# Kernel optimization log

Hardware: AMD Instinct MI355X
Metric: run time of the kernel (lower is better)

The kernel has to match this reference:

```python
import jax, jax.numpy as jnp
import numpy as np

N, H, DK, DV, DFF, D = 2, 8, 32, 32, 512, 256
B, S = 2, 2048
MASK_VALUE = -1e-30
EPS = 1e-14  # K.epsilon()**2 with default epsilon 1e-7


def glorot(key, shape):
    fan_in, fan_out = shape[-2], shape[-1]
    limit = np.sqrt(6.0 / (fan_in + fan_out))
    return jax.random.uniform(key, shape, jnp.float32, -limit, limit)


def setup_inputs() -> dict:
    key = jax.random.key(0)
    ks = jax.random.split(key, 8)
    return {
        "x": jax.random.normal(ks[0], (B, S, D), jnp.float32),
        "mask": jnp.ones((B, S), jnp.float32),
        "Wq": glorot(ks[1], (N, H, D, DK)),
        "Wk": glorot(ks[2], (N, H, D, DK)),
        "Wv": glorot(ks[3], (N, H, D, DV)),
        "Wo": glorot(ks[4], (N, H * DV, D)),
        "W1": glorot(ks[5], (N, D, DFF)),
        "b1": jnp.zeros((N, DFF), jnp.float32),
        "W2": glorot(ks[6], (N, DFF, D)),
        "b2": jnp.zeros((N, D), jnp.float32),
        "gamma": jnp.ones((2 * N,), jnp.float32),
        "beta": jnp.zeros((2 * N,), jnp.float32),
    }


def _layernorm(x, g, b):
    mean = jnp.mean(x, axis=-1, keepdims=True)
    var = jnp.mean(jnp.square(x - mean), axis=-1, keepdims=True)
    return (x - mean) / jnp.sqrt(var + EPS) * g + b


def reference(x, mask, Wq, Wk, Wv, Wo, W1, b1, W2, b2, gamma, beta):
    m = mask[:, None, None, :]  # [B,1,1,S], multiplies score rows' key axis
    for i in range(N):
        # batched multi-head attention (no 1/sqrt(dk) scaling, faithful to source)
        q = jnp.einsum("bsd,hdk->bhsk", x, Wq[i])
        k = jnp.einsum("bsd,hdk->bhsk", x, Wk[i])
        v = jnp.einsum("bsd,hdv->bhsv", x, Wv[i])
        A = jnp.einsum("bhsk,bhtk->bhst", q, k)  # [B,H,S,S]
        A = m * A + (1.0 - m) * MASK_VALUE
        A = jax.nn.softmax(A, axis=-1)
        o = jnp.einsum("bhst,bhtv->bhsv", A, v)
        conc = o.transpose(0, 2, 1, 3).reshape(x.shape[0], x.shape[1], H * DV)
        x = x + conc @ Wo[i]
        x = _layernorm(x, gamma[2 * i], beta[2 * i])
        ffn = jax.nn.relu(x @ W1[i] + b1[i]) @ W2[i] + b2[i]
        x = x + ffn
        x = _layernorm(x, gamma[2 * i + 1], beta[2 * i + 1])
    return x
```

## Files before the change

### kernel.cpp

```cpp
#include <hip/hip_runtime.h>
#include <hip/hip_bf16.h>

#define NL 2
#define NH 8
#define DKk 32
#define DVv 32
#define DFF 512
#define DD 256
#define BB 2
#define SS 2048
#define MROWS (BB*SS)
#define LN_EPS 1e-14f
#define L2E 1.4426950408889634f
#define SOFT_SHIFT_L2E (50.0f*L2E)

typedef __hip_bfloat16 bf16;
typedef unsigned short us;
typedef short bf16x8 __attribute__((ext_vector_type(8)));
typedef float f32x4  __attribute__((ext_vector_type(4)));
typedef unsigned short us4 __attribute__((ext_vector_type(4)));

#define O_XF   256
#define O_QB   (O_XF+1048576)
#define O_KH   (O_QB+1048576)
#define O_KL   (O_KH+524288)
#define O_VT   (O_KL+524288)
#define O_XH   (O_VT+524288)
#define O_XL   (O_XH+524288)
#define O_OP   (O_XL+524288)
#define O_ML   (O_OP+2097152)
#define O_MASK (O_ML+65536)
#define O_B1   (O_MASK+4096)
#define O_B2   (O_B1+1024)
#define O_GM   (O_B2+512)
#define O_BT   (O_GM+4)
#define O_PREP (O_BT+4)
#define TAIL_TOTAL (4096+1024+512+4+4)
#define CONV_BLOCKS (512 + (TAIL_TOTAL+255)/256)
#define PREP_BLOCKS 512
#define PQH 0u
#define PQL 393216u
#define POH 786432u
#define POL 917504u
#define P1H 1048576u
#define P1L 1310720u
#define P2H 1572864u
#define P2L 1835008u

__device__ __forceinline__ float us2f(us u){
  unsigned int v = ((unsigned int)u) << 16; float f;
  __builtin_memcpy(&f, &v, 4); return f;
}
__device__ __forceinline__ us f2bf_rne(float f){
  unsigned int b = __float_as_uint(f);
  b += 0x7FFFu + ((b>>16)&1u);
  return (us)(b>>16);
}

#if __has_builtin(__builtin_amdgcn_exp2f)
#define EXP2F(x) __builtin_amdgcn_exp2f(x)
#else
#define EXP2F(x) exp2f(x)
#endif

#if __has_builtin(__builtin_amdgcn_cvt_pk_bf16_f32)
typedef __bf16 bf16x2_t __attribute__((ext_vector_type(2)));
__device__ __forceinline__ int pack_bf16(float a, float b){
  bf16x2_t r = __builtin_amdgcn_cvt_pk_bf16_f32(a, b);
  int i; __builtin_memcpy(&i, &r, 4); return i;
}
#else
__device__ __forceinline__ int pack_bf16(float a, float b){
  int b0 = __float_as_int(a) + 0x8000;
  int b1 = __float_as_int(b) + 0x8000;
  return (b1 & 0xFFFF0000) | ((int)((unsigned)b0 >> 16));
}
#endif

__device__ __forceinline__ void gl_lds16(const us* g, us* l){
  __builtin_amdgcn_global_load_lds(
    (const __attribute__((address_space(1))) unsigned int*)g,
    (__attribute__((address_space(3))) unsigned int*)l, 16, 0, 0);
}

__device__ __forceinline__ size_t xhl_idx(int row, int col){
  int rt = row>>6, rg = (row>>4)&3, L15 = row&15;
  int kc = col>>5, Q = (col>>3)&3, j = col&7;
  return ((size_t)(rt*8+kc))*2048 + rg*512 + Q*128 + L15*8 + j;
}

__device__ __forceinline__ float conv1(const void* src, size_t i, int flag){
  if(flag) return ((const float*)src)[i];
  return us2f(((const us*)src)[i]);
}

__device__ __forceinline__ void prep_b_raw(const void* W0, const void* W1v, const void* W2v,
                                           int baseoff, us* __restrict__ Bh, us* __restrict__ Bl,
                                           int Kd, int Nd, int qkv, int g, int flag)
{
  int total = (Kd/32)*(Nd/16)*64;
  if(g >= total) return;
  int lane = g & 63, fi = g >> 6;
  int ncN = Nd/16;
  int nc = fi % ncN, kc = fi / ncN;
  int Q = lane>>4, L15 = lane&15;
  int n = nc*16 + L15;
  const void* src;
  int off0, stride;
  if(qkv){
    int sec = n>>8, h = (n>>5)&7, kq = n&31;
    src = (sec==0)?W0:((sec==1)?W1v:W2v);
    off0 = baseoff + h*8192 + kq;
    stride = 32;
  } else {
    src = W0;
    off0 = baseoff + n;
    stride = Nd;
  }
  #pragma unroll
  for(int j=0;j<8;j++){
    int k = kc*32 + Q*8 + j;
    float v = conv1(src, (size_t)off0 + (size_t)k*stride, flag);
    us hb = f2bf_rne(v);
    Bh[(size_t)g*8 + j] = hb;
    Bl[(size_t)g*8 + j] = f2bf_rne(v - us2f(hb));
  }
}

__global__ void conv_prep(const void* s0, const void* s1, const void* sWq, const void* sWk,
                          const void* sWv, const void* sWo, const void* sW1, const void* sb1,
                          const void* sW2, const void* sb2, const void* sgm, const void* sbt,
                          float* __restrict__ ws, int* __restrict__ flagp)
{
  __shared__ int fsh[4];
  int bad = 0;
  const us* xr = (const us*)s0;
  for(int i=threadIdx.x; i<4096; i+=256){
    float f = us2f(xr[i]);
    if(!(fabsf(f) < 1e3f)) bad = 1;
  }
  unsigned long long m = __ballot(bad);
  if((threadIdx.x&63)==0) fsh[threadIdx.x>>6] = (m!=0ull);
  __syncthreads();
  int flag = (fsh[0]|fsh[1]|fsh[2]|fsh[3]);
  if(blockIdx.x==0 && threadIdx.x==0) *flagp = flag;

  int b = blockIdx.x;
  if(b < PREP_BLOCKS){
    int layer = b >> 8, lb = b & 255;
    us* prep = (us*)(ws + O_PREP);
    if(lb < 96){
      int g = lb*256 + threadIdx.x;
      prep_b_raw(sWq, sWk, sWv, layer*65536, prep+PQH+(size_t)layer*196608,
                 prep+PQL+(size_t)layer*196608, 256, 768, 1, g, flag);
    } else if(lb < 128){
      int g = (lb-96)*256 + threadIdx.x;
      prep_b_raw(sWo, nullptr, nullptr, layer*65536, prep+POH+(size_t)layer*65536,
                 prep+POL+(size_t)layer*65536, 256, 256, 0, g, flag);
    } else if(lb < 192){
      int g = (lb-128)*256 + threadIdx.x;
      prep_b_raw(sW1, nullptr, nullptr, layer*131072, prep+P1H+(size_t)layer*131072,
                 prep+P1L+(size_t)layer*131072, 256, 512, 0, g, flag);
    } else {
      int g = (lb-192)*256 + threadIdx.x;
      prep_b_raw(sW2, nullptr, nullptr, layer*131072, prep+P2H+(size_t)layer*131072,
                 prep+P2L+(size_t)layer*131072, 512, 256, 0, g, flag);
    }
    return;
  }
  int b2 = b - PREP_BLOCKS;
  if(b2 < 512){
    int g8 = b2*256 + threadIdx.x;
    int e0 = g8*8;
    float v[8];
    if(flag){
      float4 a0 = *((const float4*)s0 + (e0>>2));
      float4 a1 = *((const float4*)s0 + (e0>>2) + 1);
      v[0]=a0.x; v[1]=a0.y; v[2]=a0.z; v[3]=a0.w;
      v[4]=a1.x; v[5]=a1.y; v[6]=a1.z; v[7]=a1.w;
    } else {
      bf16x8 u = *((const bf16x8*)s0 + g8);
      #pragma unroll
      for(int j=0;j<8;j++) v[j] = us2f((us)u[j]);
    }
    *(float4*)&ws[O_XF+e0]   = (float4){v[0],v[1],v[2],v[3]};
    *(float4*)&ws[O_XF+e0+4] = (float4){v[4],v[5],v[6],v[7]};
    union{ us a[8]; uint4 q; } hh, ll;
    #pragma unroll
    for(int j=0;j<8;j++){
      us hb = f2bf_rne(v[j]);
      hh.a[j] = hb;
      ll.a[j] = f2bf_rne(v[j] - us2f(hb));
    }
    size_t xi = xhl_idx(e0>>8, e0&255);
    *(uint4*)&((us*)(ws+O_XH))[xi] = hh.q;
    *(uint4*)&((us*)(ws+O_XL))[xi] = ll.q;
    return;
  }
  int g = (b2-512)*256 + threadIdx.x;
  if(g < 4096){ ws[O_MASK+g] = conv1(s1, g, flag)*L2E; return; }
  g -= 4096;
  if(g < 1024){ ws[O_B1+g] = conv1(sb1, g, flag); return; }
  g -= 1024;
  if(g < 512){ ws[O_B2+g] = conv1(sb2, g, flag); return; }
  g -= 512;
  if(g < 4){ ws[O_GM+g] = conv1(sgm, g, flag); return; }
  g -= 4;
  if(g < 4){ ws[O_BT+g] = conv1(sbt, g, flag); return; }
}

template<int MODE>
__launch_bounds__(256)
__global__ void gemm_mfma(const us* __restrict__ Axh, const us* __restrict__ Axl,
                          const us* __restrict__ Bh, const us* __restrict__ Bl,
                          const float* __restrict__ bias,
                          float* __restrict__ O,
                          us* __restrict__ QH, us* __restrict__ QL,
                          us* __restrict__ KH, us* __restrict__ KL, us* __restrict__ VT,
                          int Ncols, int Kdim)
{
  __shared__ __align__(16) us SH[16384];
  const int t = threadIdx.x;
  const int w = t>>6, lane = t&63;
  const int Q = lane>>4, L15 = lane&15;
  const int bx = blockIdx.x, by = blockIdx.y;
  const int row0 = bx*64;
  const int nc0 = by*4;
  const int col0 = by*64;
  const int nKc = Kdim>>5;
  const int ncW = Ncols>>4;

  f32x4 acc[2][2];
  #pragma unroll
  for(int i=0;i<2;i++)
    #pragma unroll
    for(int j=0;j<2;j++) acc[i][j] = (f32x4){0.f,0.f,0.f,0.f};

  auto stage = [&](int kc){
    const int bo = (kc&1)*8192;
    size_t abase = ((size_t)(bx*nKc + kc))*2048;
    gl_lds16(&Axh[abase + (size_t)t*8], &SH[bo + t*8]);
    gl_lds16(&Axl[abase + (size_t)t*8], &SH[bo + 2048 + t*8]);
    size_t gidx = ((size_t)(kc*ncW + nc0 + w)*64 + lane)*8;
    gl_lds16(&Bh[gidx], &SH[bo + 4096 + t*8]);
    gl_lds16(&Bl[gidx], &SH[bo + 6144 + t*8]);
  };

  stage(0);

  for(int kc=0; kc<nKc; kc++){
    __syncthreads();
    if(kc+1 < nKc) stage(kc+1);
    const int bo = (kc&1)*8192;
    const us* Ah  = SH + bo;
    const us* Al  = SH + bo + 2048;
    const us* Bhs = SH + bo + 4096;
    const us* Bls = SH + bo + 6144;

    bf16x8 aAh[2], aAl[2], bBh[2], bBl[2];
    #pragma unroll
    for(int rg2=0;rg2<2;rg2++){
      int rg = (w&1)*2 + rg2;
      aAh[rg2] = *(const bf16x8*)&Ah[rg*512 + lane*8];
      aAl[rg2] = *(const bf16x8*)&Al[rg*512 + lane*8];
    }
    #pragma unroll
    for(int cg2=0;cg2<2;cg2++){
      int nc = (w>>1)*2 + cg2;
      bBh[cg2] = *(const bf16x8*)&Bhs[nc*512 + lane*8];
      bBl[cg2] = *(const bf16x8*)&Bls[nc*512 + lane*8];
    }
    #pragma unroll
    for(int rg2=0;rg2<2;rg2++)
      #pragma unroll
      for(int cg2=0;cg2<2;cg2++){
        acc[rg2][cg2] = __builtin_amdgcn_mfma_f32_16x16x32_bf16(aAl[rg2], bBh[cg2], acc[rg2][cg2], 0,0,0);
        acc[rg2][cg2] = __builtin_amdgcn_mfma_f32_16x16x32_bf16(aAh[rg2], bBl[cg2], acc[rg2][cg2], 0,0,0);
        acc[rg2][cg2] = __builtin_amdgcn_mfma_f32_16x16x32_bf16(aAh[rg2], bBh[cg2], acc[rg2][cg2], 0,0,0);
      }
  }

  if(MODE==0){
    __syncthreads();
    us* TH = SH;
    us* TL = SH + 4608;
    #pragma unroll
    for(int rg2=0;rg2<2;rg2++)
      #pragma unroll
      for(int cg2=0;cg2<2;cg2++)
        #pragma unroll
        for(int r=0;r<4;r++){
          int rl = (w&1)*32 + rg2*16 + Q*4 + r;
          int cl = (w>>1)*32 + cg2*16 + L15;
          float va = acc[rg2][cg2][r];
          us hb = f2bf_rne(va);
          TH[rl*72+cl] = hb;
          TL[rl*72+cl] = f2bf_rne(va - us2f(hb));
        }
    __syncthreads();
    const int sec = col0>>8;
    const int h0  = (col0&255)>>5;
    const int b_  = row0>>11;
    const int srow0 = row0 & 2047;
    if(sec < 2){
      us* DH = (sec==0) ? QH : KH;
      us* DL = (sec==0) ? QL : KL;
      #pragma unroll
      for(int u2=0; u2<2; u2++){
        int u = w + u2*4;
        int rg = u&3, half = u>>2;
        int lbase = (rg*16 + L15)*72 + half*32 + Q*8;
        bf16x8 hv = *(const bf16x8*)&TH[lbase];
        bf16x8 lv = *(const bf16x8*)&TL[lbase];
        int bh = b_*NH + h0 + half;
        size_t dbase = ((size_t)(bh*128 + (srow0>>4) + rg)*64 + lane)*8;
        *(bf16x8*)&DH[dbase] = hv;
        *(bf16x8*)&DL[dbase] = lv;
      }
    } else {
      #pragma unroll
      for(int u2=0; u2<2; u2++){
        int u = w + u2*4;
        int sgrp = u&1, kqh = (u>>1)&1, half = u>>2;
        union{ us u8[8]; bf16x8 v; } vv;
        #pragma unroll
        for(int j=0;j<8;j++){
          int rl = sgrp*32 + Q*8 + j;
          int cl = half*32 + kqh*16 + L15;
          vv.u8[j] = TH[rl*72+cl];
        }
        int bh = b_*NH + h0 + half;
        size_t dbase = ((size_t)((bh*64 + (srow0>>5) + sgrp)*2 + kqh)*64 + lane)*8;
        *(bf16x8*)&VT[dbase] = vv.v;
      }
    }
  } else {
    #pragma unroll
    for(int rg2=0;rg2<2;rg2++)
      #pragma unroll
      for(int cg2=0;cg2<2;cg2++)
        #pragma unroll
        for(int r=0;r<4;r++){
          int row = row0 + (w&1)*32 + rg2*16 + Q*4 + r;
          int c   = col0 + (w>>1)*32 + cg2*16 + L15;
          float v = acc[rg2][cg2][r] + bias[c];
          O[(size_t)row*Ncols + c] = v>0.f ? v : 0.f;
        }
  }
}

__launch_bounds__(256)
__global__ void oln_ffn(const float* __restrict__ OpartA, const float* __restrict__ MLA,
                        const us* __restrict__ WOh, const us* __restrict__ WOl,
                        const us* __restrict__ W1h, const us* __restrict__ W1l,
                        const us* __restrict__ W2h, const us* __restrict__ W2l,
                        const float* __restrict__ b1, const float* __restrict__ b2,
                        float* __restrict__ xf, us* __restrict__ xh, us* __restrict__ xl,
                        const float* __restrict__ gamma, const float* __restrict__ beta, int gi0,
                        void* __restrict__ out, int write_out, const int* __restrict__ flagp)
{
  __shared__ __align__(16) us xAH[4096], xAL[4096];
  __shared__ __align__(16) us hAH[8192], hAL[8192];
  __shared__ float lred[128];
  const int t = threadIdx.x;
  const int w = t>>6, lane = t&63;
  const int Q = lane>>4, L15 = lane&15;
  const int row0 = blockIdx.x*16;
  const int b_ = row0>>11, s0_ = row0&2047;

  f32x4 acc[4];
  #pragma unroll
  for(int cg=0;cg<4;cg++) acc[cg] = (f32x4){0.f,0.f,0.f,0.f};

  #pragma unroll 2
  for(int kc=0; kc<8; kc++){
    size_t i0 = ((size_t)(b_*8 + kc))*2048 + s0_ + L15;
    float l0 = MLA[i0], l1 = MLA[i0+32768];
    float inv = 1.f/(l0 + l1);
    const float* p0 = &OpartA[i0*32 + Q*8];
    const float* p1 = &OpartA[(i0+32768)*32 + Q*8];
    float4 a0 = *(const float4*)p0, a1 = *(const float4*)(p0+4);
    float4 c0 = *(const float4*)p1, c1 = *(const float4*)(p1+4);
    float fv[8];
    fv[0]=(a0.x+c0.x)*inv; fv[1]=(a0.y+c0.y)*inv; fv[2]=(a0.z+c0.z)*inv; fv[3]=(a0.w+c0.w)*inv;
    fv[4]=(a1.x+c1.x)*inv; fv[5]=(a1.y+c1.y)*inv; fv[6]=(a1.z+c1.z)*inv; fv[7]=(a1.w+c1.w)*inv;
    union{ us a[8]; bf16x8 v; } Ahv, Alv;
    #pragma unroll
    for(int j=0;j<8;j++){
      us hb = f2bf_rne(fv[j]);
      Ahv.a[j] = hb;
      Alv.a[j] = f2bf_rne(fv[j] - us2f(hb));
    }
    #pragma unroll
    for(int cg=0;cg<4;cg++){
      size_t fi = (size_t)(kc*16 + w*4 + cg)*512 + (size_t)lane*8;
      bf16x8 bBh = *(const bf16x8*)&WOh[fi];
      bf16x8 bBl = *(const bf16x8*)&WOl[fi];
      acc[cg] = __builtin_amdgcn_mfma_f32_16x16x32_bf16(Alv.v, bBh, acc[cg], 0,0,0);
      acc[cg] = __builtin_amdgcn_mfma_f32_16x16x32_bf16(Ahv.v, bBl, acc[cg], 0,0,0);
      acc[cg] = __builtin_amdgcn_mfma_f32_16x16x32_bf16(Ahv.v, bBh, acc[cg], 0,0,0);
    }
  }

  float tmp[4][4];
  #pragma unroll
  for(int cg=0;cg<4;cg++)
    #pragma unroll
    for(int r=0;r<4;r++){
      int row = row0 + Q*4 + r;
      int c = w*64 + cg*16 + L15;
      tmp[cg][r] = acc[cg][r] + xf[(size_t)row*DD + c];
    }
  float s[4], sq[4];
  #pragma unroll
  for(int r=0;r<4;r++){
    s[r]  = tmp[0][r]+tmp[1][r]+tmp[2][r]+tmp[3][r];
    sq[r] = tmp[0][r]*tmp[0][r]+tmp[1][r]*tmp[1][r]+tmp[2][r]*tmp[2][r]+tmp[3][r]*tmp[3][r];
  }
  #pragma unroll
  for(int off=1; off<16; off<<=1)
    #pragma unroll
    for(int r=0;r<4;r++){
      s[r]  += __shfl_xor(s[r], off);
      sq[r] += __shfl_xor(sq[r], off);
    }
  if(L15==0){
    #pragma unroll
    for(int r=0;r<4;r++){
      int rl = Q*4 + r;
      lred[(w*16 + rl)*2]   = s[r];
      lred[(w*16 + rl)*2+1] = sq[r];
    }
  }
  __syncthreads();
  float val_s[4][4];
  {
    float g = gamma[gi0], bb = beta[gi0];
    float scv[4], mnv[4];
    #pragma unroll
    for(int r=0;r<4;r++){
      int rl = Q*4 + r;
      float S  = lred[rl*2]   + lred[(16+rl)*2]   + lred[(32+rl)*2]   + lred[(48+rl)*2];
      float SQ = lred[rl*2+1] + lred[(16+rl)*2+1] + lred[(32+rl)*2+1] + lred[(48+rl)*2+1];
      float mean = S*(1.f/DD);
      float var  = SQ*(1.f/DD) - mean*mean;
      scv[r] = rsqrtf(var+LN_EPS)*g;
      mnv[r] = mean;
    }
    #pragma unroll
    for(int cg=0;cg<4;cg++){
      int c = w*64 + cg*16 + L15;
      int base = (c>>5)*512 + (((c&31)>>3))*128 + (c&7);
      #pragma unroll
      for(int r=0;r<4;r++){
        float v = (tmp[cg][r]-mnv[r])*scv[r] + bb;
        val_s[cg][r] = v;
        us hb = f2bf_rne(v);
        xAH[base + (Q*4+r)*8] = hb;
        xAL[base + (Q*4+r)*8] = f2bf_rne(v - us2f(hb));
      }
    }
  }
  __syncthreads();

  #pragma unroll
  for(int nch=0; nch<2; nch++){
    f32x4 acc_h[4];
    #pragma unroll
    for(int cg=0;cg<4;cg++) acc_h[cg] = (f32x4){0.f,0.f,0.f,0.f};
    #pragma unroll 2
    for(int kc=0; kc<8; kc++){
      bf16x8 aAh = *(const bf16x8*)&xAH[kc*512 + lane*8];
      bf16x8 aAl = *(const bf16x8*)&xAL[kc*512 + lane*8];
      #pragma unroll
      for(int cg=0;cg<4;cg++){
        size_t fi = (size_t)(kc*32 + nch*16 + w*4 + cg)*512 + (size_t)lane*8;
        bf16x8 bBh = *(const bf16x8*)&W1h[fi];
        bf16x8 bBl = *(const bf16x8*)&W1l[fi];
        acc_h[cg] = __builtin_amdgcn_mfma_f32_16x16x32_bf16(aAl, bBh, acc_h[cg], 0,0,0);
        acc_h[cg] = __builtin_amdgcn_mfma_f32_16x16x32_bf16(aAh, bBl, acc_h[cg], 0,0,0);
        acc_h[cg] = __builtin_amdgcn_mfma_f32_16x16x32_bf16(aAh, bBh, acc_h[cg], 0,0,0);
      }
    }
    #pragma unroll
    for(int cg=0;cg<4;cg++){
      int col = nch*256 + (w*4+cg)*16 + L15;
      float bv = b1[col];
      int base = (col>>5)*512 + (((col&31)>>3))*128 + (col&7);
      #pragma unroll
      for(int r=0;r<4;r++){
        int row = Q*4 + r;
        float v = acc_h[cg][r] + bv;
        v = v>0.f ? v : 0.f;
        us hb = f2bf_rne(v);
        hAH[base + row*8] = hb;
        hAL[base + row*8] = f2bf_rne(v - us2f(hb));
      }
    }
  }
  __syncthreads();

  f32x4 acc_y[4];
  #pragma unroll
  for(int cg=0;cg<4;cg++) acc_y[cg] = (f32x4){0.f,0.f,0.f,0.f};
  #pragma unroll 2
  for(int kc2=0; kc2<16; kc2++){
    bf16x8 aAh = *(const bf16x8*)&hAH[kc2*512 + lane*8];
    bf16x8 aAl = *(const bf16x8*)&hAL[kc2*512 + lane*8];
    #pragma unroll
    for(int cg=0;cg<4;cg++){
      size_t fi = (size_t)(kc2*16 + w*4 + cg)*512 + (size_t)lane*8;
      bf16x8 bBh = *(const bf16x8*)&W2h[fi];
      bf16x8 bBl = *(const bf16x8*)&W2l[fi];
      acc_y[cg] = __builtin_amdgcn_mfma_f32_16x16x32_bf16(aAl, bBh, acc_y[cg], 0,0,0);
      acc_y[cg] = __builtin_amdgcn_mfma_f32_16x16x32_bf16(aAh, bBl, acc_y[cg], 0,0,0);
      acc_y[cg] = __builtin_amdgcn_mfma_f32_16x16x32_bf16(aAh, bBh, acc_y[cg], 0,0,0);
    }
  }

  float tmp2[4][4];
  #pragma unroll
  for(int cg=0;cg<4;cg++)
    #pragma unroll
    for(int r=0;r<4;r++){
      int c = w*64 + cg*16 + L15;
      tmp2[cg][r] = acc_y[cg][r] + val_s[cg][r] + b2[c];
    }
  float s2[4], sq2[4];
  #pragma unroll
  for(int r=0;r<4;r++){
    s2[r]  = tmp2[0][r]+tmp2[1][r]+tmp2[2][r]+tmp2[3][r];
    sq2[r] = tmp2[0][r]*tmp2[0][r]+tmp2[1][r]*tmp2[1][r]+tmp2[2][r]*tmp2[2][r]+tmp2[3][r]*tmp2[3][r];
  }
  #pragma unroll
  for(int off=1; off<16; off<<=1)
    #pragma unroll
    for(int r=0;r<4;r++){
      s2[r]  += __shfl_xor(s2[r], off);
      sq2[r] += __shfl_xor(sq2[r], off);
    }
  __syncthreads();
  if(L15==0){
    #pragma unroll
    for(int r=0;r<4;r++){
      int rl = Q*4 + r;
      lred[(w*16 + rl)*2]   = s2[r];
      lred[(w*16 + rl)*2+1] = sq2[r];
    }
  }
  __syncthreads();
  float g2 = gamma[gi0+1], bb2 = beta[gi0+1];
  float scv2[4], mnv2[4];
  #pragma unroll
  for(int r=0;r<4;r++){
    int rl = Q*4 + r;
    float S  = lred[rl*2]   + lred[(16+rl)*2]   + lred[(32+rl)*2]   + lred[(48+rl)*2];
    float SQ = lred[rl*2+1] + lred[(16+rl)*2+1] + lred[(32+rl)*2+1] + lred[(48+rl)*2+1];
    float mean = S*(1.f/DD);
    float var  = SQ*(1.f/DD) - mean*mean;
    scv2[r] = rsqrtf(var+LN_EPS)*g2;
    mnv2[r] = mean;
  }
  int flag = write_out ? *flagp : 0;
  #pragma unroll
  for(int cg=0;cg<4;cg++)
    #pragma unroll
    for(int r=0;r<4;r++){
      int row = row0 + Q*4 + r;
      int c = w*64 + cg*16 + L15;
      float val = (tmp2[cg][r]-mnv2[r])*scv2[r] + bb2;
      xf[(size_t)row*DD + c] = val;
      us hb = f2bf_rne(val);
      size_t xi = xhl_idx(row, c);
      xh[xi] = hb;
      xl[xi] = f2bf_rne(val - us2f(hb));
      if(write_out){
        if(flag) ((float*)out)[(size_t)row*DD + c] = val;
        else     ((bf16*)out)[(size_t)row*DD + c] = __float2bfloat16(val);
      }
    }
}

__launch_bounds__(256)
__global__ void attn_kernel(const us* __restrict__ QH, const us* __restrict__ QL,
                            const us* __restrict__ KH, const us* __restrict__ KL,
                            const us* __restrict__ VT,
                            const float* __restrict__ mask,
                            float* __restrict__ Opart, float* __restrict__ ML)
{
  __shared__ __align__(16) us Khs[4096], Kls[4096], Vts[4096];
  __shared__ __align__(16) float Msl[1024];
  const int t = threadIdx.x;
  const int bh = blockIdx.x >> 6;
  const int qt = (blockIdx.x & 63) >> 1;
  const int ks = blockIdx.x & 1;
  const int b_ = bh >> 3;
  const int wv = t >> 6;
  const int lane = t & 63;
  const int Q = lane >> 4, L15 = lane & 15;
  const int q0 = qt*64 + wv*16;

  size_t qidx = ((size_t)(bh*128 + qt*4 + wv)*64 + lane)*8;
  const bf16x8 qh_v = *(const bf16x8*)&QH[qidx];
  const bf16x8 ql_v = *(const bf16x8*)&QL[qidx];

  const us* KHbh = KH + (size_t)bh*65536;
  const us* KLbh = KL + (size_t)bh*65536;
  const us* VTbh = VT + (size_t)bh*65536;
  const int base = ks*1024;

  f32x4 Oa0a = {0.f,0.f,0.f,0.f}, Oa0b = {0.f,0.f,0.f,0.f};
  f32x4 Oa1a = {0.f,0.f,0.f,0.f}, Oa1b = {0.f,0.f,0.f,0.f};
  float lacc = 0.f;

  {
    const us* mrow = (const us*)(mask + (size_t)b_*SS + base);
    gl_lds16(mrow + (size_t)t*8, ((us*)Msl) + t*8);
    size_t kbase = (size_t)(base>>4)*512;
    size_t vbase = (size_t)(base>>5)*1024;
    gl_lds16(&KHbh[kbase + (size_t)t*8], &Khs[t*8]);
    gl_lds16(&KLbh[kbase + (size_t)t*8], &Kls[t*8]);
    gl_lds16(&VTbh[vbase + (size_t)t*8], &Vts[t*8]);
  }

  for(int s=0; s<16; s++){
    __syncthreads();
    if(s < 15){
      int t0n = base + (s+1)*64;
      int bn = (s+1)&1;
      size_t kbase = (size_t)(t0n>>4)*512;
      size_t vbase = (size_t)(t0n>>5)*1024;
      gl_lds16(&KHbh[kbase + (size_t)t*8], &Khs[bn*2048 + t*8]);
      gl_lds16(&KLbh[kbase + (size_t)t*8], &Kls[bn*2048 + t*8]);
      gl_lds16(&VTbh[vbase + (size_t)t*8], &Vts[bn*2048 + t*8]);
    }
    const int bo = (s&1)*2048;
    const int mo = s*64;

    f32x4 St[4];
    const f32x4 zz = {0.f,0.f,0.f,0.f};
    #pragma unroll
    for(int kt=0;kt<4;kt++){
      bf16x8 aKh = *(const bf16x8*)&Khs[bo + kt*512 + lane*8];
      bf16x8 aKl = *(const bf16x8*)&Kls[bo + kt*512 + lane*8];
      f32x4 a = __builtin_amdgcn_mfma_f32_16x16x32_bf16(aKl, qh_v, zz, 0,0,0);
      a = __builtin_amdgcn_mfma_f32_16x16x32_bf16(aKh, ql_v, a, 0,0,0);
      a = __builtin_amdgcn_mfma_f32_16x16x32_bf16(aKh, qh_v, a, 0,0,0);
      St[kt] = a;
    }

    float lsum = 0.f;
    #pragma unroll
    for(int kt=0;kt<4;kt++){
      float4 mv = *(const float4*)&Msl[mo + kt*16 + Q*4];
      float mvr[4] = {mv.x, mv.y, mv.z, mv.w};
      #pragma unroll
      for(int r=0;r<4;r++){
        float p = EXP2F(fmaf(mvr[r], St[kt][r], -SOFT_SHIFT_L2E));
        St[kt][r] = p;
        lsum += p;
      }
    }
    lacc += lsum;

    int pk[4][2];
    #pragma unroll
    for(int kt=0;kt<4;kt++){
      pk[kt][0] = pack_bf16(St[kt][0], St[kt][1]);
      pk[kt][1] = pack_bf16(St[kt][2], St[kt][3]);
    }

    #pragma unroll
    for(int c=0;c<2;c++){
      union { int i[4]; bf16x8 v; } bu;
      #pragma unroll
      for(int d=0;d<4;d++){
        int srcl = (((Q&1)*2 + (d>>1))<<4) | L15;
        int vlo = __shfl(pk[2*c  ][d&1], srcl, 64);
        int vhi = __shfl(pk[2*c+1][d&1], srcl, 64);
        bu.i[d] = (Q & 2) ? vhi : vlo;
      }
      bf16x8 aV0 = *(const bf16x8*)&Vts[bo + (c*2+0)*512 + lane*8];
      bf16x8 aV1 = *(const bf16x8*)&Vts[bo + (c*2+1)*512 + lane*8];
      if(c == 0){
        Oa0a = __builtin_amdgcn_mfma_f32_16x16x32_bf16(aV0, bu.v, Oa0a, 0,0,0);
        Oa1a = __builtin_amdgcn_mfma_f32_16x16x32_bf16(aV1, bu.v, Oa1a, 0,0,0);
      } else {
        Oa0b = __builtin_amdgcn_mfma_f32_16x16x32_bf16(aV0, bu.v, Oa0b, 0,0,0);
        Oa1b = __builtin_amdgcn_mfma_f32_16x16x32_bf16(aV1, bu.v, Oa1b, 0,0,0);
      }
    }
  }

  f32x4 Oa0 = Oa0a + Oa0b;
  f32x4 Oa1 = Oa1a + Oa1b;
  lacc += __shfl_xor(lacc, 16);
  lacc += __shfl_xor(lacc, 32);

  float* opp = &Opart[((size_t)(ks*16+bh)*SS + q0 + L15)*32];
  #pragma unroll
  for(int r=0;r<4;r++){
    opp[Q*4+r]    = Oa0[r];
    opp[16+Q*4+r] = Oa1[r];
  }
  if(Q==0){
    ML[(size_t)(ks*16+bh)*SS + q0 + L15] = lacc;
  }
}

extern "C" void kernel_launch(void* const* d_in, const int* in_sizes, int n_in,
                              void* d_out, int out_size, void* d_ws, size_t ws_size,
                              hipStream_t stream)
{
  float* ws = (float*)d_ws;
  int* flagp = (int*)d_ws;

  float* xf  = ws + O_XF;
  us* QHb = (us*)(ws + O_QB);
  us* QLb = QHb + 1048576;
  us* KH = (us*)(ws + O_KH);
  us* KL = (us*)(ws + O_KL);
  us* VT = (us*)(ws + O_VT);
  us* XH = (us*)(ws + O_XH);
  us* XL = (us*)(ws + O_XL);
  float* Opart = ws + O_OP;
  float* ML  = ws + O_ML;
  float* b1f = ws + O_B1;
  float* b2f_ = ws + O_B2;
  float* gmf = ws + O_GM;
  float* btf = ws + O_BT;
  us* prep = (us*)(ws + O_PREP);

  conv_prep<<<PREP_BLOCKS+CONV_BLOCKS,256,0,stream>>>(
      d_in[0], d_in[1], d_in[2], d_in[3], d_in[4], d_in[5],
      d_in[6], d_in[7], d_in[8], d_in[9], d_in[10], d_in[11],
      ws, flagp);

  for(int i=0;i<NL;i++){
    const float* b1i = b1f + (size_t)i*DFF;
    const float* b2i = b2f_ + (size_t)i*DD;

    dim3 g0(64, 12);
    gemm_mfma<0><<<g0,256,0,stream>>>(XH, XL,
                                      prep+PQH+(size_t)i*196608, prep+PQL+(size_t)i*196608,
                                      nullptr, nullptr,
                                      QHb, QLb, KH, KL, VT, 768, 256);
    attn_kernel<<<1024,256,0,stream>>>(QHb, QLb, KH, KL, VT, ws + O_MASK, Opart, ML);
    oln_ffn<<<256,256,0,stream>>>(Opart, ML,
                                  prep+POH+(size_t)i*65536, prep+POL+(size_t)i*65536,
                                  prep+P1H+(size_t)i*131072, prep+P1L+(size_t)i*131072,
                                  prep+P2H+(size_t)i*131072, prep+P2L+(size_t)i*131072,
                                  b1i, b2i, xf, XH, XL,
                                  gmf, btf, 2*i, d_out, (i==NL-1)?1:0, flagp);
  }
}
```

Before: 265.1 us.

## Widen oln_ffn to 8 waves and software-pipeline weight and attention-output loads

The fused output-projection/LayerNorm/FFN kernel now launches 512 threads per block, so each wave owns 2 instead of 4 column groups. The LayerNorm reductions are extended to combine partial sums from 8 waves. Weight fragments for the WO, W1 and W2 GEMMs are prefetched into a 4-deep register ring, and the partial attention outputs are double-buffered, so global loads overlap the MFMA work. This targets poor latency hiding in a kernel that runs only one block per CU. In exchange, the 512-thread launch bound caps registers per thread, each wave reloads the same attention rows, and one __syncthreads before the second reduction write is dropped.

```diff
diff --git a/kernel.cpp b/kernel.cpp
--- a/kernel.cpp
+++ b/kernel.cpp
@@ -77,6 +77,10 @@
 }
 #endif
 
+__device__ __forceinline__ f32x4 MF(bf16x8 a, bf16x8 b, f32x4 c){
+  return __builtin_amdgcn_mfma_f32_16x16x32_bf16(a,b,c,0,0,0);
+}
+
 __device__ __forceinline__ void gl_lds16(const us* g, us* l){
   __builtin_amdgcn_global_load_lds(
     (const __attribute__((address_space(1))) unsigned int*)g,
@@ -274,9 +278,9 @@
     for(int rg2=0;rg2<2;rg2++)
       #pragma unroll
       for(int cg2=0;cg2<2;cg2++){
-        acc[rg2][cg2] = __builtin_amdgcn_mfma_f32_16x16x32_bf16(aAl[rg2], bBh[cg2], acc[rg2][cg2], 0,0,0);
-        acc[rg2][cg2] = __builtin_amdgcn_mfma_f32_16x16x32_bf16(aAh[rg2], bBl[cg2], acc[rg2][cg2], 0,0,0);
-        acc[rg2][cg2] = __builtin_amdgcn_mfma_f32_16x16x32_bf16(aAh[rg2], bBh[cg2], acc[rg2][cg2], 0,0,0);
+        acc[rg2][cg2] = MF(aAl[rg2], bBh[cg2], acc[rg2][cg2]);
+        acc[rg2][cg2] = MF(aAh[rg2], bBl[cg2], acc[rg2][cg2]);
+        acc[rg2][cg2] = MF(aAh[rg2], bBh[cg2], acc[rg2][cg2]);
       }
   }
 
@@ -349,7 +353,7 @@
   }
 }
 
-__launch_bounds__(256)
+__launch_bounds__(512)
 __global__ void oln_ffn(const float* __restrict__ OpartA, const float* __restrict__ MLA,
                         const us* __restrict__ WOh, const us* __restrict__ WOl,
                         const us* __restrict__ W1h, const us* __restrict__ W1l,
@@ -361,61 +365,102 @@
 {
   __shared__ __align__(16) us xAH[4096], xAL[4096];
   __shared__ __align__(16) us hAH[8192], hAL[8192];
-  __shared__ float lred[128];
+  __shared__ float lred[256];
   const int t = threadIdx.x;
   const int w = t>>6, lane = t&63;
   const int Q = lane>>4, L15 = lane&15;
   const int row0 = blockIdx.x*16;
   const int b_ = row0>>11, s0_ = row0&2047;
 
-  f32x4 acc[4];
-  #pragma unroll
-  for(int cg=0;cg<4;cg++) acc[cg] = (f32x4){0.f,0.f,0.f,0.f};
-
-  #pragma unroll 2
-  for(int kc=0; kc<8; kc++){
-    size_t i0 = ((size_t)(b_*8 + kc))*2048 + s0_ + L15;
-    float l0 = MLA[i0], l1 = MLA[i0+32768];
-    float inv = 1.f/(l0 + l1);
+  bf16x8 Wh[4][2], Wl[4][2];
+  float4 Ar[2][4];
+  float  Ml[2][2];
+
+  auto loadWO_ = [&](int kc, int set){
+    #pragma unroll
+    for(int cg=0;cg<2;cg++){
+      size_t fi = (size_t)(kc*16 + w*2 + cg)*512 + (size_t)lane*8;
+      Wh[set][cg] = *(const bf16x8*)&WOh[fi];
+      Wl[set][cg] = *(const bf16x8*)&WOl[fi];
+    }
+  };
+  auto loadW1_ = [&](int nch, int kc, int set){
+    #pragma unroll
+    for(int cg=0;cg<2;cg++){
+      size_t fi = (size_t)(kc*32 + nch*16 + w*2 + cg)*512 + (size_t)lane*8;
+      Wh[set][cg] = *(const bf16x8*)&W1h[fi];
+      Wl[set][cg] = *(const bf16x8*)&W1l[fi];
+    }
+  };
+  auto loadW2_ = [&](int kc, int set){
+    #pragma unroll
+    for(int cg=0;cg<2;cg++){
+      size_t fi = (size_t)(kc*16 + w*2 + cg)*512 + (size_t)lane*8;
+      Wh[set][cg] = *(const bf16x8*)&W2h[fi];
+      Wl[set][cg] = *(const bf16x8*)&W2l[fi];
+    }
+  };
+  auto loadAr = [&](int kc, int set){
+    size_t i0 = ((size_t)(b_*8+kc))*2048 + s0_ + L15;
+    Ml[set][0] = MLA[i0]; Ml[set][1] = MLA[i0+32768];
     const float* p0 = &OpartA[i0*32 + Q*8];
     const float* p1 = &OpartA[(i0+32768)*32 + Q*8];
-    float4 a0 = *(const float4*)p0, a1 = *(const float4*)(p0+4);
-    float4 c0 = *(const float4*)p1, c1 = *(const float4*)(p1+4);
+    Ar[set][0] = *(const float4*)p0; Ar[set][1] = *(const float4*)(p0+4);
+    Ar[set][2] = *(const float4*)p1; Ar[set][3] = *(const float4*)(p1+4);
+  };
+
+  f32x4 accA[2];
+  accA[0] = accA[1] = (f32x4){0.f,0.f,0.f,0.f};
+
+  auto stepA = [&](int aset, int wset){
+    float inv = 1.f/(Ml[aset][0] + Ml[aset][1]);
     float fv[8];
-    fv[0]=(a0.x+c0.x)*inv; fv[1]=(a0.y+c0.y)*inv; fv[2]=(a0.z+c0.z)*inv; fv[3]=(a0.w+c0.w)*inv;
-    fv[4]=(a1.x+c1.x)*inv; fv[5]=(a1.y+c1.y)*inv; fv[6]=(a1.z+c1.z)*inv; fv[7]=(a1.w+c1.w)*inv;
-    union{ us a[8]; bf16x8 v; } Ahv, Alv;
+    fv[0]=(Ar[aset][0].x+Ar[aset][2].x)*inv; fv[1]=(Ar[aset][0].y+Ar[aset][2].y)*inv;
+    fv[2]=(Ar[aset][0].z+Ar[aset][2].z)*inv; fv[3]=(Ar[aset][0].w+Ar[aset][2].w)*inv;
+    fv[4]=(Ar[aset][1].x+Ar[aset][3].x)*inv; fv[5]=(Ar[aset][1].y+Ar[aset][3].y)*inv;
+    fv[6]=(Ar[aset][1].z+Ar[aset][3].z)*inv; fv[7]=(Ar[aset][1].w+Ar[aset][3].w)*inv;
+    union{ us a[8]; bf16x8 v; } Ah_, Al_;
     #pragma unroll
     for(int j=0;j<8;j++){
       us hb = f2bf_rne(fv[j]);
-      Ahv.a[j] = hb;
-      Alv.a[j] = f2bf_rne(fv[j] - us2f(hb));
-    }
-    #pragma unroll
-    for(int cg=0;cg<4;cg++){
-      size_t fi = (size_t)(kc*16 + w*4 + cg)*512 + (size_t)lane*8;
-      bf16x8 bBh = *(const bf16x8*)&WOh[fi];
-      bf16x8 bBl = *(const bf16x8*)&WOl[fi];
-      acc[cg] = __builtin_amdgcn_mfma_f32_16x16x32_bf16(Alv.v, bBh, acc[cg], 0,0,0);
-      acc[cg] = __builtin_amdgcn_mfma_f32_16x16x32_bf16(Ahv.v, bBl, acc[cg], 0,0,0);
-      acc[cg] = __builtin_amdgcn_mfma_f32_16x16x32_bf16(Ahv.v, bBh, acc[cg], 0,0,0);
-    }
-  }
-
-  float tmp[4][4];
-  #pragma unroll
-  for(int cg=0;cg<4;cg++)
+      Ah_.a[j] = hb;
+      Al_.a[j] = f2bf_rne(fv[j] - us2f(hb));
+    }
+    accA[0] = MF(Al_.v, Wh[wset][0], accA[0]);
+    accA[0] = MF(Ah_.v, Wl[wset][0], accA[0]);
+    accA[0] = MF(Ah_.v, Wh[wset][0], accA[0]);
+    accA[1] = MF(Al_.v, Wh[wset][1], accA[1]);
+    accA[1] = MF(Ah_.v, Wl[wset][1], accA[1]);
+    accA[1] = MF(Ah_.v, Wh[wset][1], accA[1]);
+  };
+
+  loadAr(0,0); loadWO_(0,0);
+  loadAr(1,1); loadWO_(1,1);
+  loadWO_(2,2); loadWO_(3,3);
+  #pragma unroll
+  for(int kc=0; kc<8; kc+=2){
+    stepA(0, kc&3);
+    if(kc+2<8) loadAr(kc+2, 0);
+    if(kc+4<8) loadWO_(kc+4, (kc+4)&3);
+    stepA(1, (kc+1)&3);
+    if(kc+3<8) loadAr(kc+3, 1);
+    if(kc+5<8) loadWO_(kc+5, (kc+5)&3);
+  }
+
+  float tmp[2][4];
+  #pragma unroll
+  for(int cg=0;cg<2;cg++)
     #pragma unroll
     for(int r=0;r<4;r++){
       int row = row0 + Q*4 + r;
-      int c = w*64 + cg*16 + L15;
-      tmp[cg][r] = acc[cg][r] + xf[(size_t)row*DD + c];
+      int c = (w*2+cg)*16 + L15;
+      tmp[cg][r] = accA[cg][r] + xf[(size_t)row*DD + c];
     }
   float s[4], sq[4];
   #pragma unroll
   for(int r=0;r<4;r++){
-    s[r]  = tmp[0][r]+tmp[1][r]+tmp[2][r]+tmp[3][r];
-    sq[r] = tmp[0][r]*tmp[0][r]+tmp[1][r]*tmp[1][r]+tmp[2][r]*tmp[2][r]+tmp[3][r]*tmp[3][r];
+    s[r]  = tmp[0][r]+tmp[1][r];
+    sq[r] = tmp[0][r]*tmp[0][r]+tmp[1][r]*tmp[1][r];
   }
   #pragma unroll
   for(int off=1; off<16; off<<=1)
@@ -433,23 +478,27 @@
     }
   }
   __syncthreads();
-  float val_s[4][4];
+  float val_s[2][4];
   {
     float g = gamma[gi0], bb = beta[gi0];
     float scv[4], mnv[4];
     #pragma unroll
     for(int r=0;r<4;r++){
       int rl = Q*4 + r;
-      float S  = lred[rl*2]   + lred[(16+rl)*2]   + lred[(32+rl)*2]   + lred[(48+rl)*2];
-      float SQ = lred[rl*2+1] + lred[(16+rl)*2+1] + lred[(32+rl)*2+1] + lred[(48+rl)*2+1];
+      float S = 0.f, SQ = 0.f;
+      #pragma unroll
+      for(int wv=0; wv<8; wv++){
+        S  += lred[(wv*16+rl)*2];
+        SQ += lred[(wv*16+rl)*2+1];
+      }
       float mean = S*(1.f/DD);
       float var  = SQ*(1.f/DD) - mean*mean;
       scv[r] = rsqrtf(var+LN_EPS)*g;
       mnv[r] = mean;
     }
     #pragma unroll
-    for(int cg=0;cg<4;cg++){
-      int c = w*64 + cg*16 + L15;
+    for(int cg=0;cg<2;cg++){
+      int c = (w*2+cg)*16 + L15;
       int base = (c>>5)*512 + (((c&31)>>3))*128 + (c&7);
       #pragma unroll
       for(int r=0;r<4;r++){
@@ -465,32 +514,33 @@
 
   #pragma unroll
   for(int nch=0; nch<2; nch++){
-    f32x4 acc_h[4];
-    #pragma unroll
-    for(int cg=0;cg<4;cg++) acc_h[cg] = (f32x4){0.f,0.f,0.f,0.f};
-    #pragma unroll 2
-    for(int kc=0; kc<8; kc++){
-      bf16x8 aAh = *(const bf16x8*)&xAH[kc*512 + lane*8];
-      bf16x8 aAl = *(const bf16x8*)&xAL[kc*512 + lane*8];
-      #pragma unroll
-      for(int cg=0;cg<4;cg++){
-        size_t fi = (size_t)(kc*32 + nch*16 + w*4 + cg)*512 + (size_t)lane*8;
-        bf16x8 bBh = *(const bf16x8*)&W1h[fi];
-        bf16x8 bBl = *(const bf16x8*)&W1l[fi];
-        acc_h[cg] = __builtin_amdgcn_mfma_f32_16x16x32_bf16(aAl, bBh, acc_h[cg], 0,0,0);
-        acc_h[cg] = __builtin_amdgcn_mfma_f32_16x16x32_bf16(aAh, bBl, acc_h[cg], 0,0,0);
-        acc_h[cg] = __builtin_amdgcn_mfma_f32_16x16x32_bf16(aAh, bBh, acc_h[cg], 0,0,0);
-      }
-    }
-    #pragma unroll
-    for(int cg=0;cg<4;cg++){
-      int col = nch*256 + (w*4+cg)*16 + L15;
+    f32x4 ah[2];
+    ah[0] = ah[1] = (f32x4){0.f,0.f,0.f,0.f};
+    loadW1_(nch,0,0); loadW1_(nch,1,1); loadW1_(nch,2,2); loadW1_(nch,3,3);
+    #pragma unroll
+    for(int kc=0; kc<8; kc+=4){
+      #pragma unroll
+      for(int sub=0; sub<4; sub++){
+        bf16x8 aAh = *(const bf16x8*)&xAH[(kc+sub)*512 + lane*8];
+        bf16x8 aAl = *(const bf16x8*)&xAL[(kc+sub)*512 + lane*8];
+        ah[0] = MF(aAl, Wh[sub][0], ah[0]);
+        ah[0] = MF(aAh, Wl[sub][0], ah[0]);
+        ah[0] = MF(aAh, Wh[sub][0], ah[0]);
+        ah[1] = MF(aAl, Wh[sub][1], ah[1]);
+        ah[1] = MF(aAh, Wl[sub][1], ah[1]);
+        ah[1] = MF(aAh, Wh[sub][1], ah[1]);
+        if(kc+sub+4 < 8) loadW1_(nch, kc+sub+4, sub);
+      }
+    }
+    #pragma unroll
+    for(int cg=0;cg<2;cg++){
+      int col = nch*256 + (w*2+cg)*16 + L15;
       float bv = b1[col];
       int base = (col>>5)*512 + (((col&31)>>3))*128 + (col&7);
       #pragma unroll
       for(int r=0;r<4;r++){
         int row = Q*4 + r;
-        float v = acc_h[cg][r] + bv;
+        float v = ah[cg][r] + bv;
         v = v>0.f ? v : 0.f;
         us hb = f2bf_rne(v);
         hAH[base + row*8] = hb;
@@ -500,37 +550,38 @@
   }
   __syncthreads();
 
-  f32x4 acc_y[4];
-  #pragma unroll
-  for(int cg=0;cg<4;cg++) acc_y[cg] = (f32x4){0.f,0.f,0.f,0.f};
-  #pragma unroll 2
-  for(int kc2=0; kc2<16; kc2++){
-    bf16x8 aAh = *(const bf16x8*)&hAH[kc2*512 + lane*8];
-    bf16x8 aAl = *(const bf16x8*)&hAL[kc2*512 + lane*8];
-    #pragma unroll
-    for(int cg=0;cg<4;cg++){
-      size_t fi = (size_t)(kc2*16 + w*4 + cg)*512 + (size_t)lane*8;
-      bf16x8 bBh = *(const bf16x8*)&W2h[fi];
-      bf16x8 bBl = *(const bf16x8*)&W2l[fi];
-      acc_y[cg] = __builtin_amdgcn_mfma_f32_16x16x32_bf16(aAl, bBh, acc_y[cg], 0,0,0);
-      acc_y[cg] = __builtin_amdgcn_mfma_f32_16x16x32_bf16(aAh, bBl, acc_y[cg], 0,0,0);
-      acc_y[cg] = __builtin_amdgcn_mfma_f32_16x16x32_bf16(aAh, bBh, acc_y[cg], 0,0,0);
-    }
-  }
-
-  float tmp2[4][4];
-  #pragma unroll
-  for(int cg=0;cg<4;cg++)
+  f32x4 ay[2];
+  ay[0] = ay[1] = (f32x4){0.f,0.f,0.f,0.f};
+  loadW2_(0,0); loadW2_(1,1); loadW2_(2,2); loadW2_(3,3);
+  #pragma unroll
+  for(int kc2=0; kc2<16; kc2+=4){
+    #pragma unroll
+    for(int sub=0; sub<4; sub++){
+      bf16x8 aAh = *(const bf16x8*)&hAH[(kc2+sub)*512 + lane*8];
+      bf16x8 aAl = *(const bf16x8*)&hAL[(kc2+sub)*512 + lane*8];
+      ay[0] = MF(aAl, Wh[sub][0], ay[0]);
+      ay[0] = MF(aAh, Wl[sub][0], ay[0]);
+      ay[0] = MF(aAh, Wh[sub][0], ay[0]);
+      ay[1] = MF(aAl, Wh[sub][1], ay[1]);
+      ay[1] = MF(aAh, Wl[sub][1], ay[1]);
+      ay[1] = MF(aAh, Wh[sub][1], ay[1]);
+      if(kc2+sub+4 < 16) loadW2_(kc2+sub+4, sub);
+    }
+  }
+
+  float tmp2[2][4];
+  #pragma unroll
+  for(int cg=0;cg<2;cg++)
     #pragma unroll
     for(int r=0;r<4;r++){
-      int c = w*64 + cg*16 + L15;
-      tmp2[cg][r] = acc_y[cg][r] + val_s[cg][r] + b2[c];
+      int c = (w*2+cg)*16 + L15;
+      tmp2[cg][r] = ay[cg][r] + val_s[cg][r] + b2[c];
     }
   float s2[4], sq2[4];
   #pragma unroll
   for(int r=0;r<4;r++){
-    s2[r]  = tmp2[0][r]+tmp2[1][r]+tmp2[2][r]+tmp2[3][r];
-    sq2[r] = tmp2[0][r]*tmp2[0][r]+tmp2[1][r]*tmp2[1][r]+tmp2[2][r]*tmp2[2][r]+tmp2[3][r]*tmp2[3][r];
+    s2[r]  = tmp2[0][r]+tmp2[1][r];
+    sq2[r] = tmp2[0][r]*tmp2[0][r]+tmp2[1][r]*tmp2[1][r];
   }
   #pragma unroll
   for(int off=1; off<16; off<<=1)
@@ -539,7 +590,6 @@
       s2[r]  += __shfl_xor(s2[r], off);
       sq2[r] += __shfl_xor(sq2[r], off);
     }
-  __syncthreads();
   if(L15==0){
     #pragma unroll
     for(int r=0;r<4;r++){
@@ -554,8 +604,12 @@
   #pragma unroll
   for(int r=0;r<4;r++){
     int rl = Q*4 + r;
-    float S  = lred[rl*2]   + lred[(16+rl)*2]   + lred[(32+rl)*2]   + lred[(48+rl)*2];
-    float SQ = lred[rl*2+1] + lred[(16+rl)*2+1] + lred[(32+rl)*2+1] + lred[(48+rl)*2+1];
+    float S = 0.f, SQ = 0.f;
+    #pragma unroll
+    for(int wv=0; wv<8; wv++){
+      S  += lred[(wv*16+rl)*2];
+      SQ += lred[(wv*16+rl)*2+1];
+    }
     float mean = S*(1.f/DD);
     float var  = SQ*(1.f/DD) - mean*mean;
     scv2[r] = rsqrtf(var+LN_EPS)*g2;
@@ -563,11 +617,11 @@
   }
   int flag = write_out ? *flagp : 0;
   #pragma unroll
-  for(int cg=0;cg<4;cg++)
+  for(int cg=0;cg<2;cg++)
     #pragma unroll
     for(int r=0;r<4;r++){
       int row = row0 + Q*4 + r;
-      int c = w*64 + cg*16 + L15;
+      int c = (w*2+cg)*16 + L15;
       float val = (tmp2[cg][r]-mnv2[r])*scv2[r] + bb2;
       xf[(size_t)row*DD + c] = val;
       us hb = f2bf_rne(val);
@@ -643,9 +697,9 @@
     for(int kt=0;kt<4;kt++){
       bf16x8 aKh = *(const bf16x8*)&Khs[bo + kt*512 + lane*8];
       bf16x8 aKl = *(const bf16x8*)&Kls[bo + kt*512 + lane*8];
-      f32x4 a = __builtin_amdgcn_mfma_f32_16x16x32_bf16(aKl, qh_v, zz, 0,0,0);
-      a = __builtin_amdgcn_mfma_f32_16x16x32_bf16(aKh, ql_v, a, 0,0,0);
-      a = __builtin_amdgcn_mfma_f32_16x16x32_bf16(aKh, qh_v, a, 0,0,0);
+      f32x4 a = MF(aKl, qh_v, zz);
+      a = MF(aKh, ql_v, a);
+      a = MF(aKh, qh_v, a);
       St[kt] = a;
     }
 
@@ -683,11 +737,11 @@
       bf16x8 aV0 = *(const bf16x8*)&Vts[bo + (c*2+0)*512 + lane*8];
       bf16x8 aV1 = *(const bf16x8*)&Vts[bo + (c*2+1)*512 + lane*8];
       if(c == 0){
-        Oa0a = __builtin_amdgcn_mfma_f32_16x16x32_bf16(aV0, bu.v, Oa0a, 0,0,0);
-        Oa1a = __builtin_amdgcn_mfma_f32_16x16x32_bf16(aV1, bu.v, Oa1a, 0,0,0);
+        Oa0a = MF(aV0, bu.v, Oa0a);
+        Oa1a = MF(aV1, bu.v, Oa1a);
       } else {
-        Oa0b = __builtin_amdgcn_mfma_f32_16x16x32_bf16(aV0, bu.v, Oa0b, 0,0,0);
-        Oa1b = __builtin_amdgcn_mfma_f32_16x16x32_bf16(aV1, bu.v, Oa1b, 0,0,0);
+        Oa0b = MF(aV0, bu.v, Oa0b);
+        Oa1b = MF(aV1, bu.v, Oa1b);
       }
     }
   }
@@ -746,7 +800,7 @@
                                       nullptr, nullptr,
                                       QHb, QLb, KH, KL, VT, 768, 256);
     attn_kernel<<<1024,256,0,stream>>>(QHb, QLb, KH, KL, VT, ws + O_MASK, Opart, ML);
-    oln_ffn<<<256,256,0,stream>>>(Opart, ML,
+    oln_ffn<<<256,512,0,stream>>>(Opart, ML,
                                   prep+POH+(size_t)i*65536, prep+POL+(size_t)i*65536,
                                   prep+P1H+(size_t)i*131072, prep+P1L+(size_t)i*131072,
                                   prep+P2H+(size_t)i*131072, prep+P2L+(size_t)i*131072,
```

Result: faster. 247.5 us (-6.6%).
